# Optimization experiments

Measured on AMD Instinct MI355X. Metric: run time of the kernel, lower is better.

Reference implementation:

```python
import jax, jax.numpy as jnp
import numpy as np

S, D, H, DI, DV, DFF = 2048, 1024, 16, 64, 64, 4096


def _xavier(k, shape):
    fan_in, fan_out = shape[-2], shape[-1]
    lim = float(np.sqrt(6.0 / (fan_in + fan_out)))
    return jax.random.uniform(k, shape, jnp.float32, -lim, lim)


def setup_inputs() -> dict:
    key = jax.random.key(0)
    ks = jax.random.split(key, 8)
    input_vecs = jax.random.normal(ks[0], (S, D), jnp.float32)
    WQs = _xavier(ks[1], (H, D, DI))
    WKs = _xavier(ks[2], (H, D, DI))
    WVs = _xavier(ks[3], (H, D, DV))
    WO_w = _xavier(ks[4], (D, H * DV))   # torch Linear weight [out, in]
    WO_b = jnp.zeros((D,), jnp.float32)
    FF1_w = _xavier(ks[5], (DFF, D))
    FF1_b = jnp.zeros((DFF,), jnp.float32)
    FF2_w = _xavier(ks[6], (D, DFF))
    FF2_b = jnp.zeros((D,), jnp.float32)
    return dict(input_vecs=input_vecs, WQs=WQs, WKs=WKs, WVs=WVs,
                WO_w=WO_w, WO_b=WO_b, FF1_w=FF1_w, FF1_b=FF1_b,
                FF2_w=FF2_w, FF2_b=FF2_b)


def reference(input_vecs, WQs, WKs, WVs, WO_w, WO_b, FF1_w, FF1_b, FF2_w, FF2_b):
    h, _, di = WQs.shape
    s = input_vecs.shape[0]
    # per-head projections: [h, s, di/dv]
    Q = jnp.einsum('sd,hde->hse', input_vecs, WQs)
    K = jnp.einsum('sd,hde->hse', input_vecs, WKs)
    V = jnp.einsum('sd,hdv->hsv', input_vecs, WVs)
    scores = jnp.einsum('hse,hte->hst', Q, K) / jnp.sqrt(jnp.float32(di))
    # ALiBi bias: slope_h = (2^{-8/H})^h for h = 1..H; bias = -max(0, i-j)*slope
    idx = jnp.arange(s)
    delta = idx[:, None] - idx[None, :]               # [s, s], i - j
    slopes = (2.0 ** (-8.0 / h)) ** jnp.arange(1, h + 1, dtype=jnp.float32)
    bias = -jnp.maximum(delta, 0).astype(jnp.float32) * slopes[:, None, None]
    causal_mask = jnp.where(delta < 0, -jnp.inf, 0.0)  # -inf above diagonal
    SA = jax.nn.softmax(scores + bias + causal_mask, axis=-1)  # [h, s, s]
    z = jnp.einsum('hst,htv->hsv', SA, V)
    # hstack over heads == transpose to [s, h, dv] then flatten
    zconcat = jnp.transpose(z, (1, 0, 2)).reshape(s, -1)
    attouts = input_vecs + zconcat @ WO_w.T + WO_b
    output_vecs = attouts + jax.nn.relu(attouts @ FF1_w.T + FF1_b) @ FF2_w.T + FF2_b
    return SA, output_vecs
```

## Files before the change

kernel.cpp:

```cpp
#include <hip/hip_runtime.h>
#include <hip/hip_bf16.h>

typedef __hip_bfloat16 bf16;
typedef short v8s __attribute__((ext_vector_type(8)));
typedef float f32x4 __attribute__((ext_vector_type(4)));

static constexpr int S = 2048, D = 1024, H = 16, DFF = 4096;

__device__ __forceinline__ bf16  f2b(float x) { return __float2bfloat16(x); }
__device__ __forceinline__ float b2f(bf16 x)  { return __bfloat162float(x); }

__device__ __forceinline__ void gl2lds16(const void* g, void* l) {
    __builtin_amdgcn_global_load_lds(
        (const __attribute__((address_space(1))) unsigned int*)g,
        (__attribute__((address_space(3))) unsigned int*)l, 16, 0, 0);
}

__global__ __launch_bounds__(256)
void prep(const float* __restrict__ X, const float* __restrict__ WO,
          const float* __restrict__ F1, const float* __restrict__ F2,
          bf16* __restrict__ Xb, bf16* __restrict__ WOb,
          bf16* __restrict__ F1b, bf16* __restrict__ F2b,
          const float* __restrict__ WQ, const float* __restrict__ WK,
          const float* __restrict__ WV, bf16* __restrict__ Wcat)
{
    __shared__ float t[64][65];
    const int bid = blockIdx.x, tid = threadIdx.x;
    if (bid < 16384) {
        const float* src; bf16* dst; int n4;
        switch (bid >> 12) {
            case 0:  src = X;  dst = Xb;  n4 = S * D / 4;   break;
            case 1:  src = WO; dst = WOb; n4 = D * D / 4;   break;
            case 2:  src = F1; dst = F1b; n4 = DFF * D / 4; break;
            default: src = F2; dst = F2b; n4 = D * DFF / 4; break;
        }
        const int i = (bid & 4095) * 256 + tid;
        if (i < n4) {
            const float4 v = ((const float4*)src)[i];
            bf16* p = dst + (size_t)i * 4;
            p[0] = f2b(v.x); p[1] = f2b(v.y); p[2] = f2b(v.z); p[3] = f2b(v.w);
        }
    } else {
        const int rem = bid - 16384;
        const int d0 = (rem & 15) * 64, h = (rem >> 4) & 15, sel = rem >> 8;
        const float* W = (sel == 0) ? WQ : (sel == 1) ? WK : WV;
        for (int idx = tid; idx < 4096; idx += 256) {
            const int d = idx >> 6, e = idx & 63;
            t[d][e] = W[((size_t)h * D + d0 + d) * 64 + e];
        }
        __syncthreads();
        for (int idx = tid; idx < 4096; idx += 256) {
            const int e = idx >> 6, d = idx & 63;
            Wcat[(size_t)(sel * 1024 + h * 64 + e) * D + d0 + d] = f2b(t[d][e]);
        }
    }
}

template<int EPI>
__global__ __launch_bounds__(256)
void gemm_nt(const bf16* __restrict__ A, const bf16* __restrict__ B,
             int M, int N, int Kd, int Kstride,
             float* __restrict__ out_f)
{
    __shared__ bf16 sA[128 * 32];
    __shared__ bf16 sB[128 * 32];
    const int tid = threadIdx.x;
    const int lane = tid & 63, quad = lane >> 4, l15 = lane & 15;
    const int wave = tid >> 6, wm = wave >> 1, wn = wave & 1;
    const size_t m0 = (size_t)blockIdx.x * 128, n0 = (size_t)blockIdx.y * 128;
    const int koff = blockIdx.z * Kd;
    const int trow = tid >> 2, tcol = (tid & 3) * 8;

    const bf16* pA = A + (m0 + trow) * (size_t)Kstride + koff + tcol;
    const bf16* pB = B + (n0 + trow) * (size_t)Kstride + koff + tcol;
    bf16* lA = sA + tid * 8;
    bf16* lB = sB + tid * 8;

    f32x4 acc[4][4] = {};

    for (int k0 = 0; k0 < Kd; k0 += 32) {
        gl2lds16(pA + k0, lA);
        gl2lds16(pA + 64 * (size_t)Kstride + k0, lA + 2048);
        gl2lds16(pB + k0, lB);
        gl2lds16(pB + 64 * (size_t)Kstride + k0, lB + 2048);
        __syncthreads();
        v8s af[4], bfr[4];
        #pragma unroll
        for (int t = 0; t < 4; ++t) {
            af[t]  = *(const v8s*)(sA + (wm * 64 + t * 16 + l15) * 32 + quad * 8);
            bfr[t] = *(const v8s*)(sB + (wn * 64 + t * 16 + l15) * 32 + quad * 8);
        }
        #pragma unroll
        for (int i = 0; i < 4; ++i)
            #pragma unroll
            for (int j = 0; j < 4; ++j)
                acc[i][j] = __builtin_amdgcn_mfma_f32_16x16x32_bf16(af[i], bfr[j], acc[i][j], 0, 0, 0);
        __syncthreads();
    }

    #pragma unroll
    for (int i = 0; i < 4; ++i) {
        const size_t mbase = m0 + wm * 64 + i * 16 + quad * 4;
        #pragma unroll
        for (int j = 0; j < 4; ++j) {
            const size_t n = n0 + wn * 64 + j * 16 + l15;
            float* po = out_f + (size_t)blockIdx.z * (size_t)M * N;
            #pragma unroll
            for (int r = 0; r < 4; ++r)
                po[(mbase + r) * (size_t)N + n] = acc[i][j][r];
        }
    }
}

template<int EPI>
__global__ __launch_bounds__(512, 2)
void gemm128n(const bf16* __restrict__ A, const bf16* __restrict__ B,
              int M, int N, int Kd, int Kstride,
              const float* __restrict__ bias,
              float* __restrict__ out_f, bf16* __restrict__ out_h,
              bf16* __restrict__ Qb, bf16* __restrict__ Kb, bf16* __restrict__ Vt)
{
    __shared__ __attribute__((aligned(16))) bf16 sA[2][128 * 64];
    __shared__ __attribute__((aligned(16))) bf16 sB[2][256 * 64];
    const int tid = threadIdx.x;
    const int lane = tid & 63, wave = tid >> 6;
    const int quad = lane >> 4, l15 = lane & 15;
    const int wm = wave >> 2, wn = wave & 3;
    const size_t m0 = (size_t)blockIdx.x * 128, n0 = (size_t)blockIdx.y * 256;
    const int koff = (EPI == 4) ? blockIdx.z * Kd : 0;
    const int NT = Kd / 64;
    const int srow = lane >> 3, schunk = lane & 7;

    f32x4 acc[4][4] = {};

#define STAGE_A(buf, tt, h)                                                    \
    {                                                                          \
        const int k0s = koff + (tt) * 64;                                      \
        const int c = wave;                                                    \
        const int r0 = (c >> 2) * 64 + (h) * 32 + (c & 3) * 8;                 \
        const int rr = r0 + srow;                                              \
        const int sc = schunk ^ (rr & 7);                                      \
        const bf16* gp = A + (m0 + (size_t)rr) * (size_t)Kstride               \
                           + k0s + sc * 8;                                     \
        gl2lds16(gp, &buf[r0 * 64] + lane * 8);                                \
    }

#define STAGE_B(buf, tt, h)                                                    \
    {                                                                          \
        const int k0s = koff + (tt) * 64;                                      \
        _Pragma("unroll")                                                      \
        for (int l = 0; l < 2; ++l) {                                          \
            const int c = wave * 2 + l;                                        \
            const int r0 = (c >> 2) * 64 + (h) * 32 + (c & 3) * 8;             \
            const int rr = r0 + srow;                                          \
            const int sc = schunk ^ (rr & 7);                                  \
            const bf16* gp = B + (n0 + (size_t)rr) * (size_t)Kstride           \
                               + k0s + sc * 8;                                 \
            gl2lds16(gp, &buf[r0 * 64] + lane * 8);                            \
        }                                                                      \
    }

#define PHASE(bufA, bufB, mh, nh, STAGE_STMT, WAIT_STMT)                       \
    {                                                                          \
        v8s af[2][2], bv[2][2];                                                \
        _Pragma("unroll")                                                      \
        for (int f = 0; f < 2; ++f)                                            \
            _Pragma("unroll")                                                  \
            for (int ks = 0; ks < 2; ++ks) {                                   \
                const int r = wm * 64 + (mh) * 32 + f * 16 + l15;              \
                const int byt = (r * 128 + ks * 64 + quad * 16) ^ ((r & 7) << 4); \
                af[f][ks] = *(const v8s*)((const char*)(bufA) + byt);          \
            }                                                                  \
        _Pragma("unroll")                                                      \
        for (int g = 0; g < 2; ++g)                                            \
            _Pragma("unroll")                                                  \
            for (int ks = 0; ks < 2; ++ks) {                                   \
                const int r = wn * 64 + (nh) * 32 + g * 16 + l15;              \
                const int byt = (r * 128 + ks * 64 + quad * 16) ^ ((r & 7) << 4); \
                bv[g][ks] = *(const v8s*)((const char*)(bufB) + byt);          \
            }                                                                  \
        STAGE_STMT;                                                            \
        __builtin_amdgcn_s_barrier();                                          \
        __builtin_amdgcn_s_setprio(1);                                         \
        _Pragma("unroll")                                                      \
        for (int ks = 0; ks < 2; ++ks)                                         \
            _Pragma("unroll")                                                  \
            for (int f = 0; f < 2; ++f)                                        \
                _Pragma("unroll")                                              \
                for (int g = 0; g < 2; ++g)                                    \
                    acc[(mh) * 2 + f][(nh) * 2 + g] =                          \
                        __builtin_amdgcn_mfma_f32_16x16x32_bf16(               \
                            af[f][ks], bv[g][ks],                              \
                            acc[(mh) * 2 + f][(nh) * 2 + g], 0, 0, 0);         \
        __builtin_amdgcn_s_setprio(0);                                         \
        WAIT_STMT;                                                             \
        __builtin_amdgcn_s_barrier();                                          \
    }

    bf16* a0 = sA[0]; bf16* a1 = sA[1];
    bf16* b0 = sB[0]; bf16* b1 = sB[1];

    STAGE_A(a0, 0, 0); STAGE_A(a0, 0, 1);
    STAGE_B(b0, 0, 0); STAGE_B(b0, 0, 1);
    STAGE_A(a1, 1, 0); STAGE_B(b1, 1, 0);
    asm volatile("s_waitcnt vmcnt(3)" ::: "memory");
    __builtin_amdgcn_s_barrier();

    for (int t = 0; t < NT; ++t) {
        bf16* cA = (t & 1) ? a1 : a0; bf16* cB = (t & 1) ? b1 : b0;
        bf16* nA = (t & 1) ? a0 : a1; bf16* nB = (t & 1) ? b0 : b1;
        const bool s1 = (t + 1 < NT), s2 = (t + 2 < NT);
        PHASE(cA, cB, 0, 0, { if (s1) STAGE_A(nA, t + 1, 1); }, {});
        PHASE(cA, cB, 0, 1, { if (s1) STAGE_B(nB, t + 1, 1); }, {});
        PHASE(cA, cB, 1, 0, { if (s2) STAGE_A(cA, t + 2, 0); }, {});
        PHASE(cA, cB, 1, 1, { if (s2) STAGE_B(cB, t + 2, 0); },
              { if (s2) { asm volatile("s_waitcnt vmcnt(3)" ::: "memory"); }
                else    { asm volatile("s_waitcnt vmcnt(0)" ::: "memory"); } });
    }
#undef PHASE
#undef STAGE_A
#undef STAGE_B

    #pragma unroll
    for (int mf = 0; mf < 4; ++mf) {
        const size_t mbase = m0 + wm * 64 + mf * 16 + quad * 4;
        #pragma unroll
        for (int nf = 0; nf < 4; ++nf) {
            const size_t n = n0 + wn * 64 + nf * 16 + l15;
            if constexpr (EPI == 0) {
                const int sel = (int)(n >> 10), hh = (int)((n >> 6) & 15), e = (int)(n & 63);
                if (sel == 2) {
                    bf16* p = Vt + ((size_t)hh * 64 + e) * S + mbase;
                    p[0] = f2b(acc[mf][nf][0]); p[1] = f2b(acc[mf][nf][1]);
                    p[2] = f2b(acc[mf][nf][2]); p[3] = f2b(acc[mf][nf][3]);
                } else {
                    const float sc = (sel == 0) ? 0.125f : 1.0f;
                    bf16* p = ((sel == 0) ? Qb : Kb) + ((size_t)hh * S + mbase) * 64 + e;
                    p[0]   = f2b(acc[mf][nf][0] * sc);
                    p[64]  = f2b(acc[mf][nf][1] * sc);
                    p[128] = f2b(acc[mf][nf][2] * sc);
                    p[192] = f2b(acc[mf][nf][3] * sc);
                }
            } else if constexpr (EPI == 2) {
                const float bval = bias[n];
                #pragma unroll
                for (int r = 0; r < 4; ++r)
                    out_h[(mbase + r) * (size_t)N + n] =
                        f2b(fmaxf(acc[mf][nf][r] + bval, 0.f));
            } else {
                float* po = out_f + (size_t)blockIdx.z * ((size_t)M * N);
                #pragma unroll
                for (int r = 0; r < 4; ++r)
                    po[(mbase + r) * (size_t)N + n] = acc[mf][nf][r];
            }
        }
    }
}

__global__ __launch_bounds__(256)
void wo_combine(const float* __restrict__ p0, const float* __restrict__ p1,
                const float* __restrict__ bias, const float* __restrict__ X,
                float* __restrict__ attf, bf16* __restrict__ atth)
{
    const int i = blockIdx.x * 256 + threadIdx.x;
    const float4 a = ((const float4*)p0)[i];
    const float4 b = ((const float4*)p1)[i];
    const float4 x = ((const float4*)X)[i];
    const float4 bs = ((const float4*)bias)[i & (D / 4 - 1)];
    float4 o;
    o.x = a.x + b.x + x.x + bs.x;
    o.y = a.y + b.y + x.y + bs.y;
    o.z = a.z + b.z + x.z + bs.z;
    o.w = a.w + b.w + x.w + bs.w;
    ((float4*)attf)[i] = o;
    bf16* ph = atth + (size_t)i * 4;
    ph[0] = f2b(o.x); ph[1] = f2b(o.y); ph[2] = f2b(o.z); ph[3] = f2b(o.w);
}

__global__ __launch_bounds__(256)
void ff2_combine4(const float* __restrict__ p0, const float* __restrict__ p1,
                  const float* __restrict__ p2, const float* __restrict__ p3,
                  const float* __restrict__ bias, const float* __restrict__ attf,
                  float* __restrict__ out2)
{
    const int i = blockIdx.x * 256 + threadIdx.x;
    const float4 a = ((const float4*)p0)[i];
    const float4 b = ((const float4*)p1)[i];
    const float4 c = ((const float4*)p2)[i];
    const float4 d = ((const float4*)p3)[i];
    const float4 r = ((const float4*)attf)[i];
    const float4 bs = ((const float4*)bias)[i & (D / 4 - 1)];
    float4 o;
    o.x = a.x + b.x + c.x + d.x + r.x + bs.x;
    o.y = a.y + b.y + c.y + d.y + r.y + bs.y;
    o.z = a.z + b.z + c.z + d.z + r.z + bs.z;
    o.w = a.w + b.w + c.w + d.w + r.w + bs.w;
    ((float4*)out2)[i] = o;
}

__global__ __launch_bounds__(512)
void attn_kernel(const bf16* __restrict__ Qb, const bf16* __restrict__ Kb,
                 const bf16* __restrict__ Vt, float* __restrict__ SA,
                 bf16* __restrict__ zf)
{
    constexpr int EST = 2056;
    __shared__ bf16 ebuf[16 * EST];
    __shared__ float wsum[8][16];
    __shared__ float inv16[16];
    __shared__ float pvacc[8][16][16];

    const int bi = (int)gridDim.x - 1 - (int)blockIdx.x;
    const int h = blockIdx.y;
    const int i0 = bi * 16;
    const int tid = threadIdx.x, wave = tid >> 6, lane = tid & 63;
    const int quad = lane >> 4, l15 = lane & 15;
    const int ntiles = bi + 1;
    const float slope = exp2f(-0.5f * (float)(h + 1));

    if (tid < 256) {
        const int r = tid >> 4, c = ntiles * 16 + (tid & 15);
        if (c < EST) ebuf[r * EST + c] = f2b(0.f);
    }

    const bf16* Qrow = Qb + ((size_t)h * S + i0 + l15) * 64;
    const v8s qf0 = *(const v8s*)(Qrow + quad * 8);
    const v8s qf1 = *(const v8s*)(Qrow + 32 + quad * 8);

    const bf16* Kh = Kb + (size_t)h * S * 64;
    float esum[4] = {0.f, 0.f, 0.f, 0.f};
    {
        int jt = wave;
        v8s kf0 = {}, kf1 = {};
        if (jt < ntiles) {
            const bf16* Krow = Kh + (size_t)(jt * 16 + l15) * 64;
            kf0 = *(const v8s*)(Krow + quad * 8);
            kf1 = *(const v8s*)(Krow + 32 + quad * 8);
        }
        while (jt < ntiles) {
            const int jn = jt + 8;
            v8s nf0 = kf0, nf1 = kf1;
            if (jn < ntiles) {
                const bf16* Krow = Kh + (size_t)(jn * 16 + l15) * 64;
                nf0 = *(const v8s*)(Krow + quad * 8);
                nf1 = *(const v8s*)(Krow + 32 + quad * 8);
            }
            f32x4 c = {0.f, 0.f, 0.f, 0.f};
            c = __builtin_amdgcn_mfma_f32_16x16x32_bf16(qf0, kf0, c, 0, 0, 0);
            c = __builtin_amdgcn_mfma_f32_16x16x32_bf16(qf1, kf1, c, 0, 0, 0);
            const int j = jt * 16 + l15;
            #pragma unroll
            for (int r = 0; r < 4; ++r) {
                const int i = i0 + quad * 4 + r;
                float e = 0.f;
                if (j <= i) e = __expf(c[r] - (float)(i - j) * slope);
                const bf16 eb = f2b(e);
                ebuf[(quad * 4 + r) * EST + j] = eb;
                esum[r] += b2f(eb);
            }
            kf0 = nf0; kf1 = nf1; jt = jn;
        }
    }
    #pragma unroll
    for (int r = 0; r < 4; ++r) {
        float v = esum[r];
        v += __shfl_xor(v, 1); v += __shfl_xor(v, 2);
        v += __shfl_xor(v, 4); v += __shfl_xor(v, 8);
        if (l15 == 0) wsum[wave][quad * 4 + r] = v;
    }
    __syncthreads();
    if (tid < 16) {
        float s = 0.f;
        #pragma unroll
        for (int w = 0; w < 8; ++w) s += wsum[w][tid];
        inv16[tid] = 1.f / s;
    }
    __syncthreads();

    {
        const int c4 = tid;
        const int nst4 = ((i0 + 15) >> 2) + 1;
        if (c4 < nst4) {
            const int col = c4 * 4;
            float* SAb = SA + ((size_t)h * S + i0) * S;
            #pragma unroll 4
            for (int row = 0; row < 16; ++row) {
                const int i = i0 + row;
                if (col <= i) {
                    const float iv = inv16[row];
                    const bf16* er = ebuf + row * EST + col;
                    float4 o;
                    o.x = b2f(er[0]) * iv;
                    o.y = (col + 1 <= i) ? b2f(er[1]) * iv : 0.f;
                    o.z = (col + 2 <= i) ? b2f(er[2]) * iv : 0.f;
                    o.w = (col + 3 <= i) ? b2f(er[3]) * iv : 0.f;
                    ((float4*)(SAb + (size_t)row * S))[c4] = o;
                }
            }
        }
    }

    const int nc = (bi + 2) >> 1;
    const int vt = wave & 3, jh = wave >> 2;
    const bf16* Vrow = Vt + ((size_t)h * 64 + vt * 16 + l15) * (size_t)S;
    f32x4 oc = {0.f, 0.f, 0.f, 0.f};
    {
        int ch = jh;
        v8s vf = {};
        if (ch < nc) vf = *(const v8s*)(Vrow + ch * 32 + quad * 8);
        while (ch < nc) {
            const int cn = ch + 2;
            v8s vn = vf;
            if (cn < nc) vn = *(const v8s*)(Vrow + cn * 32 + quad * 8);
            const v8s pf = *(const v8s*)(ebuf + l15 * EST + ch * 32 + quad * 8);
            oc = __builtin_amdgcn_mfma_f32_16x16x32_bf16(pf, vf, oc, 0, 0, 0);
            vf = vn; ch = cn;
        }
    }
    #pragma unroll
    for (int r = 0; r < 4; ++r)
        pvacc[wave][quad * 4 + r][l15] = oc[r];
    __syncthreads();
    for (int idx = tid; idx < 1024; idx += 512) {
        const int v4 = idx >> 8, rem = idx & 255, row = rem >> 4, col = rem & 15;
        const float z = (pvacc[v4][row][col] + pvacc[v4 + 4][row][col]) * inv16[row];
        zf[(size_t)(i0 + row) * (H * 64) + h * 64 + v4 * 16 + col] = f2b(z);
    }
}

extern "C" void kernel_launch(void* const* d_in, const int* in_sizes, int n_in,
                              void* d_out, int out_size, void* d_ws, size_t ws_size,
                              hipStream_t stream)
{
    const float* X     = (const float*)d_in[0];
    const float* WQs   = (const float*)d_in[1];
    const float* WKs   = (const float*)d_in[2];
    const float* WVs   = (const float*)d_in[3];
    const float* WO_w  = (const float*)d_in[4];
    const float* WO_b  = (const float*)d_in[5];
    const float* FF1_w = (const float*)d_in[6];
    const float* FF1_b = (const float*)d_in[7];
    const float* FF2_w = (const float*)d_in[8];
    const float* FF2_b = (const float*)d_in[9];

    float* SA   = (float*)d_out;
    float* out2 = SA + (size_t)H * S * S;

    char* ws = (char*)d_ws;
    const size_t MB = 1u << 20;
    bf16*  FF1b = (bf16*)(ws);
    bf16*  FF2b = (bf16*)(ws + 8 * MB);
    bf16*  Xb   = (bf16*)(ws + 16 * MB);
    bf16*  Wcat = (bf16*)(ws + 20 * MB);
    bf16*  WOb  = (bf16*)(ws + 26 * MB);
    bf16*  zf   = (bf16*)(ws + 28 * MB);
    bf16*  Qb   = (bf16*)(ws + 32 * MB);
    bf16*  Kb   = (bf16*)(ws + 36 * MB);
    bf16*  Vt   = (bf16*)(ws + 40 * MB);
    float* attf = (float*)(ws + 44 * MB);
    bf16*  atth = (bf16*)(ws + 52 * MB);
    bf16*  y1   = (bf16*)(ws + 56 * MB);
    float* pW   = (float*)(ws + 72 * MB);

    const size_t SD = (size_t)S * D;

    prep<<<dim3(16384 + 768), 256, 0, stream>>>(X, WO_w, FF1_w, FF2_w,
        Xb, WOb, FF1b, FF2b, WQs, WKs, WVs, Wcat);
    gemm128n<0><<<dim3(16, 12), 512, 0, stream>>>(Xb, Wcat, S, 3072, D, D,
        nullptr, nullptr, nullptr, Qb, Kb, Vt);
    attn_kernel<<<dim3(S / 16, H), 512, 0, stream>>>(Qb, Kb, Vt, SA, zf);
    gemm_nt<4><<<dim3(16, 8, 2), 256, 0, stream>>>(zf, WOb, S, D, D / 2, D, pW);
    wo_combine<<<dim3(S * D / 4 / 256), 256, 0, stream>>>(
        pW, pW + SD, WO_b, X, attf, atth);
    gemm128n<2><<<dim3(16, 16), 512, 0, stream>>>(atth, FF1b, S, DFF, D, D,
        FF1_b, nullptr, y1, nullptr, nullptr, nullptr);
    gemm128n<4><<<dim3(16, 4, 4), 512, 0, stream>>>(y1, FF2b, S, D, DFF / 4, DFF,
        nullptr, pW, nullptr, nullptr, nullptr, nullptr);
    ff2_combine4<<<dim3(S * D / 4 / 256), 256, 0, stream>>>(
        pW, pW + SD, pW + 2 * SD, pW + 3 * SD, FF2_b, attf, out2);
}
```

Baseline: 506.6 us.

## Drop split-K for WO and FF2 GEMMs, fuse bias/residual epilogues

Removes split-K partial buffers and the separate combine kernels for the WO projection and FF2 GEMMs, and folds bias plus residual addition (and the bf16 copy) into the GEMM epilogue. The WO GEMM now uses the larger 128x256 pipelined kernel instead of the simple gemm_nt. This removes two kernel launches and the fp32 partial write/read traffic. In exchange the grids shrink to 64 blocks each with full-K loops, which leaves many CUs idle on a large GPU.

```diff
diff --git a/kernel.cpp b/kernel.cpp
--- a/kernel.cpp
+++ b/kernel.cpp
@@ -57,66 +57,10 @@
 }
 
 template<int EPI>
-__global__ __launch_bounds__(256)
-void gemm_nt(const bf16* __restrict__ A, const bf16* __restrict__ B,
-             int M, int N, int Kd, int Kstride,
-             float* __restrict__ out_f)
-{
-    __shared__ bf16 sA[128 * 32];
-    __shared__ bf16 sB[128 * 32];
-    const int tid = threadIdx.x;
-    const int lane = tid & 63, quad = lane >> 4, l15 = lane & 15;
-    const int wave = tid >> 6, wm = wave >> 1, wn = wave & 1;
-    const size_t m0 = (size_t)blockIdx.x * 128, n0 = (size_t)blockIdx.y * 128;
-    const int koff = blockIdx.z * Kd;
-    const int trow = tid >> 2, tcol = (tid & 3) * 8;
-
-    const bf16* pA = A + (m0 + trow) * (size_t)Kstride + koff + tcol;
-    const bf16* pB = B + (n0 + trow) * (size_t)Kstride + koff + tcol;
-    bf16* lA = sA + tid * 8;
-    bf16* lB = sB + tid * 8;
-
-    f32x4 acc[4][4] = {};
-
-    for (int k0 = 0; k0 < Kd; k0 += 32) {
-        gl2lds16(pA + k0, lA);
-        gl2lds16(pA + 64 * (size_t)Kstride + k0, lA + 2048);
-        gl2lds16(pB + k0, lB);
-        gl2lds16(pB + 64 * (size_t)Kstride + k0, lB + 2048);
-        __syncthreads();
-        v8s af[4], bfr[4];
-        #pragma unroll
-        for (int t = 0; t < 4; ++t) {
-            af[t]  = *(const v8s*)(sA + (wm * 64 + t * 16 + l15) * 32 + quad * 8);
-            bfr[t] = *(const v8s*)(sB + (wn * 64 + t * 16 + l15) * 32 + quad * 8);
-        }
-        #pragma unroll
-        for (int i = 0; i < 4; ++i)
-            #pragma unroll
-            for (int j = 0; j < 4; ++j)
-                acc[i][j] = __builtin_amdgcn_mfma_f32_16x16x32_bf16(af[i], bfr[j], acc[i][j], 0, 0, 0);
-        __syncthreads();
-    }
-
-    #pragma unroll
-    for (int i = 0; i < 4; ++i) {
-        const size_t mbase = m0 + wm * 64 + i * 16 + quad * 4;
-        #pragma unroll
-        for (int j = 0; j < 4; ++j) {
-            const size_t n = n0 + wn * 64 + j * 16 + l15;
-            float* po = out_f + (size_t)blockIdx.z * (size_t)M * N;
-            #pragma unroll
-            for (int r = 0; r < 4; ++r)
-                po[(mbase + r) * (size_t)N + n] = acc[i][j][r];
-        }
-    }
-}
-
-template<int EPI>
 __global__ __launch_bounds__(512, 2)
 void gemm128n(const bf16* __restrict__ A, const bf16* __restrict__ B,
               int M, int N, int Kd, int Kstride,
-              const float* __restrict__ bias,
+              const float* __restrict__ bias, const float* __restrict__ res_f,
               float* __restrict__ out_f, bf16* __restrict__ out_h,
               bf16* __restrict__ Qb, bf16* __restrict__ Kb, bf16* __restrict__ Vt)
 {
@@ -127,7 +71,7 @@
     const int quad = lane >> 4, l15 = lane & 15;
     const int wm = wave >> 2, wn = wave & 3;
     const size_t m0 = (size_t)blockIdx.x * 128, n0 = (size_t)blockIdx.y * 256;
-    const int koff = (EPI == 4) ? blockIdx.z * Kd : 0;
+    const int koff = 0;
     const int NT = Kd / 64;
     const int srow = lane >> 3, schunk = lane & 7;
 
@@ -241,6 +185,15 @@
                     p[128] = f2b(acc[mf][nf][2] * sc);
                     p[192] = f2b(acc[mf][nf][3] * sc);
                 }
+            } else if constexpr (EPI == 1) {
+                const float bval = bias[n];
+                #pragma unroll
+                for (int r = 0; r < 4; ++r) {
+                    const size_t m = mbase + r;
+                    const float v = acc[mf][nf][r] + bval + res_f[m * (size_t)N + n];
+                    out_f[m * (size_t)N + n] = v;
+                    out_h[m * (size_t)N + n] = f2b(v);
+                }
             } else if constexpr (EPI == 2) {
                 const float bval = bias[n];
                 #pragma unroll
@@ -248,54 +201,16 @@
                     out_h[(mbase + r) * (size_t)N + n] =
                         f2b(fmaxf(acc[mf][nf][r] + bval, 0.f));
             } else {
-                float* po = out_f + (size_t)blockIdx.z * ((size_t)M * N);
+                const float bval = bias[n];
                 #pragma unroll
-                for (int r = 0; r < 4; ++r)
-                    po[(mbase + r) * (size_t)N + n] = acc[mf][nf][r];
+                for (int r = 0; r < 4; ++r) {
+                    const size_t m = mbase + r;
+                    out_f[m * (size_t)N + n] =
+                        acc[mf][nf][r] + bval + res_f[m * (size_t)N + n];
+                }
             }
         }
     }
-}
-
-__global__ __launch_bounds__(256)
-void wo_combine(const float* __restrict__ p0, const float* __restrict__ p1,
-                const float* __restrict__ bias, const float* __restrict__ X,
-                float* __restrict__ attf, bf16* __restrict__ atth)
-{
-    const int i = blockIdx.x * 256 + threadIdx.x;
-    const float4 a = ((const float4*)p0)[i];
-    const float4 b = ((const float4*)p1)[i];
-    const float4 x = ((const float4*)X)[i];
-    const float4 bs = ((const float4*)bias)[i & (D / 4 - 1)];
-    float4 o;
-    o.x = a.x + b.x + x.x + bs.x;
-    o.y = a.y + b.y + x.y + bs.y;
-    o.z = a.z + b.z + x.z + bs.z;
-    o.w = a.w + b.w + x.w + bs.w;
-    ((float4*)attf)[i] = o;
-    bf16* ph = atth + (size_t)i * 4;
-    ph[0] = f2b(o.x); ph[1] = f2b(o.y); ph[2] = f2b(o.z); ph[3] = f2b(o.w);
-}
-
-__global__ __launch_bounds__(256)
-void ff2_combine4(const float* __restrict__ p0, const float* __restrict__ p1,
-                  const float* __restrict__ p2, const float* __restrict__ p3,
-                  const float* __restrict__ bias, const float* __restrict__ attf,
-                  float* __restrict__ out2)
-{
-    const int i = blockIdx.x * 256 + threadIdx.x;
-    const float4 a = ((const float4*)p0)[i];
-    const float4 b = ((const float4*)p1)[i];
-    const float4 c = ((const float4*)p2)[i];
-    const float4 d = ((const float4*)p3)[i];
-    const float4 r = ((const float4*)attf)[i];
-    const float4 bs = ((const float4*)bias)[i & (D / 4 - 1)];
-    float4 o;
-    o.x = a.x + b.x + c.x + d.x + r.x + bs.x;
-    o.y = a.y + b.y + c.y + d.y + r.y + bs.y;
-    o.z = a.z + b.z + c.z + d.z + r.z + bs.z;
-    o.w = a.w + b.w + c.w + d.w + r.w + bs.w;
-    ((float4*)out2)[i] = o;
 }
 
 __global__ __launch_bounds__(512)
@@ -459,22 +374,16 @@
     float* attf = (float*)(ws + 44 * MB);
     bf16*  atth = (bf16*)(ws + 52 * MB);
     bf16*  y1   = (bf16*)(ws + 56 * MB);
-    float* pW   = (float*)(ws + 72 * MB);
-
-    const size_t SD = (size_t)S * D;
 
     prep<<<dim3(16384 + 768), 256, 0, stream>>>(X, WO_w, FF1_w, FF2_w,
         Xb, WOb, FF1b, FF2b, WQs, WKs, WVs, Wcat);
     gemm128n<0><<<dim3(16, 12), 512, 0, stream>>>(Xb, Wcat, S, 3072, D, D,
-        nullptr, nullptr, nullptr, Qb, Kb, Vt);
+        nullptr, nullptr, nullptr, nullptr, Qb, Kb, Vt);
     attn_kernel<<<dim3(S / 16, H), 512, 0, stream>>>(Qb, Kb, Vt, SA, zf);
-    gemm_nt<4><<<dim3(16, 8, 2), 256, 0, stream>>>(zf, WOb, S, D, D / 2, D, pW);
-    wo_combine<<<dim3(S * D / 4 / 256), 256, 0, stream>>>(
-        pW, pW + SD, WO_b, X, attf, atth);
+    gemm128n<1><<<dim3(16, 4), 512, 0, stream>>>(zf, WOb, S, D, D, D,
+        WO_b, X, attf, atth, nullptr, nullptr, nullptr);
     gemm128n<2><<<dim3(16, 16), 512, 0, stream>>>(atth, FF1b, S, DFF, D, D,
-        FF1_b, nullptr, y1, nullptr, nullptr, nullptr);
-    gemm128n<4><<<dim3(16, 4, 4), 512, 0, stream>>>(y1, FF2b, S, D, DFF / 4, DFF,
-        nullptr, pW, nullptr, nullptr, nullptr, nullptr);
-    ff2_combine4<<<dim3(S * D / 4 / 256), 256, 0, stream>>>(
-        pW, pW + SD, pW + 2 * SD, pW + 3 * SD, FF2_b, attf, out2);
-}
+        FF1_b, nullptr, nullptr, y1, nullptr, nullptr, nullptr);
+    gemm128n<3><<<dim3(16, 4), 512, 0, stream>>>(y1, FF2b, S, D, DFF, DFF,
+        FF2_b, attf, out2, nullptr, nullptr, nullptr, nullptr);
+}
```

Measured after the change: 561.0 us. 10.7% more time.
